# Kernel optimization log

Hardware: AMD Instinct MI355X
Metric: run time of the kernel (lower is better)

Reference implementation:

```python
import jax, jax.numpy as jnp
import numpy as np
from jax import lax

DEPTH = 8
LEAK = 0.01  # activations.relu(x, 0.01) == leaky relu


def _lrelu(z):
    return jnp.where(z >= 0, z, LEAK * z)


def _forward(x, mask, bucket_size, W_emb, b_emb, W, U, b, W1, b1,
             W_action_1, U_action_1, b_action_1, W_action_3, b_action_3):
    S = int(bucket_size)
    B = x.shape[0]
    H = W_emb.shape[1]
    dm = mask.T[:S]                         # [S,B] data mask (float)
    xe = x @ W_emb + b_emb                  # [B,S,H] embedding
    xe = jnp.transpose(xe, (1, 0, 2))[:S]   # [S,B,H] time-major
    # last_value_mask: 1 only at the final time step
    lvm = jnp.concatenate([jnp.zeros((S - 1, B), jnp.float32),
                           jnp.ones((1, B), jnp.float32)], axis=0)

    def hstep(carry, seq):
        h_tm1, nm_tm1, hv_tm1 = carry
        xt, pm, phv, lv = seq
        # action MLP -> per-sample gate
        a = _lrelu(xt @ W_action_1 + h_tm1 @ U_action_1 + b_action_1)  # [B,A]
        nm = jnp.clip(0.2 * (a @ W_action_3 + b_action_3) + 0.5, 0.0, 1.0)[:, 0]  # hard_sigmoid
        nm = (1.0 - lv) * (pm * phv * nm)
        both = pm * phv * (1.0 - nm) * hv_tm1
        x_only = pm * phv * (nm + (1.0 - nm) * (1.0 - hv_tm1))
        h_only = (1.0 - pm + pm * (1.0 - phv)) * (1.0 - nm) * hv_tm1
        hv = both + x_only + h_only
        h_ = _lrelu(xt @ W + h_tm1 @ U + b)      # [B,inner]
        h_ = _lrelu(h_ @ W1 + b1)                # [B,H]
        h = both[:, None] * h_ + x_only[:, None] * xt + h_only[:, None] * h_tm1
        return (h, nm, hv), (h, nm, hv)

    def vstep(carry, _):
        xv, xm, phv = carry  # [S,B,H], [S,B], [S,B]
        init = (jnp.zeros((B, H), jnp.float32),
                jnp.ones((B,), jnp.float32),
                jnp.zeros((B,), jnp.float32))
        _, (hs, nms, hvs) = lax.scan(hstep, init, (xv, xm, phv, lvm))
        # shift new_mask left by one step, pad last step with ones
        nms = jnp.concatenate([nms[1:], jnp.ones((1, B), jnp.float32)], axis=0)
        return (hs, nms, hvs), None

    (hfin, _, _), _ = lax.scan(vstep, (xe, dm, dm), None, length=DEPTH - 1)
    return hfin[-1]  # [B,H]: last time step of the last vertical level


def setup_inputs() -> dict:
    key = jax.random.key(0)
    ks = jax.random.split(key, 9)
    B, S, IN, H, INNER, A = 64, 256, 256, 256, 512, 64
    g = lambda k, shp: jax.random.normal(k, shp, jnp.float32) * np.float32(np.sqrt(2.0 / (shp[0] + shp[1])))
    return {
        "x": jax.random.normal(ks[0], (B, S, IN), jnp.float32),
        "mask": jnp.ones((B, S), jnp.float32),
        "bucket_size": S,
        "W_emb": g(ks[1], (IN, H)),
        "b_emb": jnp.zeros((H,), jnp.float32),
        "W": g(ks[2], (H, INNER)),
        "U": g(ks[3], (H, INNER)),
        "b": jnp.zeros((INNER,), jnp.float32),
        "W1": g(ks[4], (INNER, H)),
        "b1": jnp.zeros((H,), jnp.float32),
        "W_action_1": g(ks[5], (H, A)),
        "U_action_1": g(ks[6], (H, A)),
        "b_action_1": jnp.zeros((A,), jnp.float32),
        "W_action_3": g(ks[7], (A, 1)),
        "b_action_3": jnp.zeros((1,), jnp.float32),
    }


def reference(x, mask, bucket_size, W_emb, b_emb, W, U, b, W1, b1,
              W_action_1, U_action_1, b_action_1, W_action_3, b_action_3):
    return _forward(x, mask, bucket_size, W_emb, b_emb, W, U, b, W1, b1,
                    W_action_1, U_action_1, b_action_1, W_action_3, b_action_3)
```

## Files before the change

### kernel.cpp

```cpp
#include <hip/hip_runtime.h>
#include <stdint.h>


typedef _Float16 f16x8 __attribute__((ext_vector_type(8)));
typedef float    f32x4 __attribute__((ext_vector_type(4)));

static constexpr int SS = 256, BB = 64, DIN = 256, DH = 256, DNN = 512, DA = 64;

static constexpr size_t OFF_FLAGS = 0;
static constexpr size_t OFF_WEMB  = 8192;
static constexpr size_t SZ_WEMB   = (size_t)DIN * DH * 2;
static constexpr size_t OFF_W     = OFF_WEMB + SZ_WEMB;
static constexpr size_t SZ_WU     = (size_t)DH * DNN * 2;
static constexpr size_t OFF_U     = OFF_W + SZ_WU;
static constexpr size_t OFF_W1    = OFF_U + SZ_WU;
static constexpr size_t SZ_W1     = (size_t)DNN * DH * 2;
static constexpr size_t OFF_WA1   = OFF_W1 + SZ_W1;
static constexpr size_t SZ_WA     = (size_t)DH * DA * 2;
static constexpr size_t OFF_UA1   = OFF_WA1 + SZ_WA;
static constexpr size_t OFF_NM    = OFF_UA1 + SZ_WA;
static constexpr size_t SZ_NM     = (size_t)SS * BB * 4;
static constexpr size_t OFF_HV    = OFF_NM + 8 * SZ_NM;
static constexpr size_t OFF_G1    = OFF_HV + 8 * SZ_NM;
static constexpr size_t SZ_G1     = (size_t)BB * DNN * 2;
static constexpr size_t OFF_Z     = OFF_G1 + 8 * SZ_G1;
static constexpr size_t OFF_HB    = (size_t)4 << 20;
static constexpr size_t SZ_HB     = (size_t)SS * BB * DH * 2;
static constexpr size_t WS_NEEDED = OFF_HB + 8 * SZ_HB;

__device__ __forceinline__ float lrelu(float v) { return v >= 0.0f ? v : 0.01f * v; }

__device__ __forceinline__ f32x4 ld128(const f32x4* p) {
  f32x4 r;
  asm volatile("global_load_dwordx4 %0, %1, off sc0 sc1" : "=v"(r) : "v"(p) : "memory");
  return r;
}
__device__ __forceinline__ void st128(f32x4* p, f32x4 v) {
  asm volatile("global_store_dwordx4 %0, %1, off sc0 sc1" :: "v"(p), "v"(v) : "memory");
}
__device__ __forceinline__ float ldf(const float* p) {
  float r;
  asm volatile("global_load_dword %0, %1, off sc0 sc1" : "=v"(r) : "v"(p) : "memory");
  return r;
}
__device__ __forceinline__ void stf(float* p, float v) {
  asm volatile("global_store_dword %0, %1, off sc0 sc1" :: "v"(p), "v"(v) : "memory");
}
__device__ __forceinline__ void vwait() { asm volatile("s_waitcnt vmcnt(0)" ::: "memory"); }

__device__ __forceinline__ void pollf(const unsigned* p, unsigned need) {
  #pragma nounroll
  for (int g = 0; g < (1 << 18); ++g) {
    unsigned v;
    asm volatile("global_load_dword %0, %1, off sc0 sc1\n\ts_waitcnt vmcnt(0)"
                 : "=v"(v) : "v"(p) : "memory");
    if (v >= need) return;
  }
}

__global__ void zero_flags_k(unsigned* f) {
  f[threadIdx.x] = 0u;
  f[threadIdx.x + 1024] = 0u;
}

__global__ void pack_weight_k(const float* __restrict__ src, _Float16* __restrict__ dst,
                              int K, int N) {
  int idx = blockIdx.x * 256 + threadIdx.x;
  if (idx >= K * N) return;
  int k = idx / N, n = idx - k * N;
  int kt = k >> 5, q = (k >> 3) & 3, jj = k & 7;
  int nt = n >> 4, l = n & 15;
  size_t p = (((size_t)(kt * (N >> 4) + nt) * 4 + q) * 16 + l) * 8 + jj;
  dst[p] = (_Float16)src[idx];
}

__global__ __launch_bounds__(512, 2) void emb_k(const float* __restrict__ xin,
                                                const float* __restrict__ b_emb,
                                                char* __restrict__ ws) {
  const int tid = threadIdx.x, wave = tid >> 6, lane = tid & 63;
  const int l15 = lane & 15, quad = lane >> 4;
  const _Float16* Wp = (const _Float16*)(ws + OFF_WEMB);
  _Float16* xe = (_Float16*)(ws + OFF_HB);

  f16x8 bE[16];
  #pragma unroll
  for (int kt = 0; kt < 8; ++kt)
    #pragma unroll
    for (int i = 0; i < 2; ++i)
      bE[kt * 2 + i] = *(const f16x8*)(Wp + (((size_t)(kt * 16 + (wave * 2 + i)) * 4 + quad) * 16 + l15) * 8);
  float ber[2] = { b_emb[(wave * 2) * 16 + l15], b_emb[(wave * 2 + 1) * 16 + l15] };

  __shared__ __align__(16) _Float16 xtF[32 * 65 * 8];
  __shared__ __align__(16) _Float16 oF[32 * 65 * 8];

  for (int tt = 0; tt < 4; ++tt) {
    const int t = (int)blockIdx.x + 64 * tt;
    #pragma unroll
    for (int c = 0; c < 4; ++c) {
      int u = tid + 512 * c, s = u >> 5, kg = u & 31;
      const float* src = xin + ((size_t)s * SS + t) * DIN + kg * 8;
      f32x4 v0 = *(const f32x4*)src, v1 = *(const f32x4*)(src + 4);
      f16x8 p;
      p[0]=(_Float16)v0[0]; p[1]=(_Float16)v0[1]; p[2]=(_Float16)v0[2]; p[3]=(_Float16)v0[3];
      p[4]=(_Float16)v1[0]; p[5]=(_Float16)v1[1]; p[6]=(_Float16)v1[2]; p[7]=(_Float16)v1[3];
      *(f16x8*)(xtF + ((size_t)kg * 65 + s) * 8) = p;
    }
    __syncthreads();
    f32x4 acc[2][4] = {};
    #pragma unroll
    for (int kt = 0; kt < 8; ++kt) {
      f16x8 ax[4];
      #pragma unroll
      for (int mt = 0; mt < 4; ++mt)
        ax[mt] = *(const f16x8*)(xtF + (((size_t)(kt * 4 + quad)) * 65 + (mt * 16 + l15)) * 8);
      #pragma unroll
      for (int i = 0; i < 2; ++i)
        #pragma unroll
        for (int mt = 0; mt < 4; ++mt)
          acc[i][mt] = __builtin_amdgcn_mfma_f32_16x16x32_f16(ax[mt], bE[kt * 2 + i], acc[i][mt], 0, 0, 0);
    }
    #pragma unroll
    for (int i = 0; i < 2; ++i) {
      int n = (wave * 2 + i) * 16 + l15;
      int kq = n >> 3, jn = n & 7;
      #pragma unroll
      for (int mt = 0; mt < 4; ++mt)
        #pragma unroll
        for (int r = 0; r < 4; ++r) {
          int s = mt * 16 + quad * 4 + r;
          oF[((size_t)kq * 65 + s) * 8 + jn] = (_Float16)(acc[i][mt][r] + ber[i]);
        }
    }
    __syncthreads();
    #pragma unroll
    for (int c = 0; c < 4; ++c) {
      int u = tid + 512 * c, kq = u >> 6, s = u & 63;
      f32x4 v = *(const f32x4*)(oF + ((size_t)kq * 65 + s) * 8);
      *((f32x4*)(xe + (((size_t)t * 32 + kq) * 64 + s) * 8)) = v;
    }
    __syncthreads();
  }
}

__global__ __launch_bounds__(512, 2) void pipe_k(
    const float* __restrict__ mask, const float* __restrict__ b_in,
    const float* __restrict__ b1v, const float* __restrict__ bA1,
    const float* __restrict__ WA3, const float* __restrict__ bA3,
    char* __restrict__ ws, float* __restrict__ outp) {
  const int level = 1 + ((int)blockIdx.x >> 3);
  const int j     = (int)blockIdx.x & 7;
  const int tid   = threadIdx.x, wave = tid >> 6, lane = tid & 63;
  const int l15   = lane & 15, quad = lane >> 4;

  unsigned* flags = (unsigned*)(ws + OFF_FLAGS);
  unsigned* hfl   = flags + level * 64;
  unsigned* hflP  = flags + (level - 1) * 64;
  unsigned* gfl   = flags + (8 + level) * 64;

  const _Float16* Wp   = (const _Float16*)(ws + OFF_W);
  const _Float16* Up   = (const _Float16*)(ws + OFF_U);
  const _Float16* W1p  = (const _Float16*)(ws + OFF_W1);
  const _Float16* WA1p = (const _Float16*)(ws + OFF_WA1);
  const _Float16* UA1p = (const _Float16*)(ws + OFF_UA1);

  const f32x4* hPrev4 = (const f32x4*)((_Float16*)(ws + OFF_HB) + (size_t)(level - 1) * SS * BB * DH);
  f32x4*       hOwn4  = (f32x4*)((_Float16*)(ws + OFF_HB) + (size_t)level * SS * BB * DH);
  f32x4*       g1g4   = (f32x4*)(ws + OFF_G1 + (size_t)level * SZ_G1);
  float*       zg     = (float*)(ws + OFF_Z + (size_t)level * 4096);
  float*       nmW    = (float*)(ws + OFF_NM + (size_t)level * SZ_NM);
  float*       hvW    = (float*)(ws + OFF_HV + (size_t)level * SZ_NM);
  const float* nmR    = (const float*)(ws + OFF_NM + (size_t)(level - 1) * SZ_NM);
  const float* hvR    = (const float*)(ws + OFF_HV + (size_t)(level - 1) * SZ_NM);

  const int ntG = j * 4 + (wave >> 1);
  const int m0  = (wave & 1) * 2;
  f16x8 bW[8], bU[8];
  #pragma unroll
  for (int kt = 0; kt < 8; ++kt) {
    bW[kt] = *(const f16x8*)(Wp + (((size_t)(kt * 32 + ntG) * 4 + quad) * 16 + l15) * 8);
    bU[kt] = *(const f16x8*)(Up + (((size_t)(kt * 32 + ntG) * 4 + quad) * 16 + l15) * 8);
  }
  const int nt1 = j * 2 + (wave & 1);
  const int mt1 = wave >> 1;
  f16x8 b1f[16];
  #pragma unroll
  for (int kt = 0; kt < 16; ++kt)
    b1f[kt] = *(const f16x8*)(W1p + (((size_t)(kt * 16 + nt1) * 4 + quad) * 16 + l15) * 8);

  const int nG = ntG * 16 + l15;
  const int nC = nt1 * 16 + l15;
  const float bir  = b_in[nG];
  const float b1r  = b1v[nC];
  const float wa3r = WA3[(j & 3) * 16 + l15];
  const float ba1r = bA1[(j & 3) * 16 + l15];
  const float bA3v = bA3[0];

  __shared__ __align__(16) _Float16 xtF[32 * 64 * 8];
  __shared__ __align__(16) _Float16 htF[32 * 64 * 8];
  __shared__ __align__(16) _Float16 g1F[64 * 64 * 8];
  __shared__ __align__(16) _Float16 waF[16 * 64 * 8];
  __shared__ float gB[64], gX[64], gH[64], gHv[64];

  if (j < 4) {
    for (int u = tid; u < 1024; u += 512) {
      int ktm = u >> 6, lu = u & 63, kt = ktm >> 1, m = ktm & 1;
      const _Float16* sp = (m ? UA1p : WA1p) +
          (((size_t)(kt * 4 + j) * 4 + (lu >> 4)) * 16 + (lu & 15)) * 8;
      *(f16x8*)(waF + (size_t)u * 8) = *(const f16x8*)sp;
    }
  }
  for (int i = tid; i < 32 * 64 * 8; i += 512) htF[i] = (_Float16)0;
  if (tid < 64) gHv[tid] = 0.0f;
  float hreg[4] = {0.f, 0.f, 0.f, 0.f};
  __syncthreads();

  if (level >= 2) pollf(hflP + wave, 1);
  __syncthreads();
  {
    f32x4 pf[4];
    #pragma unroll
    for (int c = 0; c < 4; ++c) pf[c] = ld128(hPrev4 + tid + 512 * c);
    vwait();
    #pragma unroll
    for (int c = 0; c < 4; ++c) ((f32x4*)xtF)[tid + 512 * c] = pf[c];
  }
  __syncthreads();

  for (int t = 0; t < SS; ++t) {
    const bool last = (t == SS - 1);

    if (t > 0) pollf(hfl + wave, (unsigned)t);
    if (level >= 2) {
      unsigned need = (unsigned)((t + 2 <= SS) ? (t + 2) : SS);
      pollf(hflP + wave, need);
    }
    if (t > 0 && wave != j) {
      const f32x4* src = hOwn4 + (size_t)(t - 1) * 2048 + wave * 256;
      f32x4 hv4[4];
      #pragma unroll
      for (int it = 0; it < 4; ++it) hv4[it] = ld128(src + it * 64 + lane);
      vwait();
      #pragma unroll
      for (int it = 0; it < 4; ++it) ((f32x4*)htF)[wave * 256 + it * 64 + lane] = hv4[it];
    }
    __syncthreads();

    {
      f32x4 a0 = {}, a1 = {};
      #pragma unroll
      for (int kt = 0; kt < 8; ++kt) {
        int kq = kt * 4 + quad;
        f16x8 ax0 = *(const f16x8*)(xtF + ((size_t)(kq * 64 + m0 * 16 + l15)) * 8);
        f16x8 ax1 = *(const f16x8*)(xtF + ((size_t)(kq * 64 + (m0 + 1) * 16 + l15)) * 8);
        f16x8 ah0 = *(const f16x8*)(htF + ((size_t)(kq * 64 + m0 * 16 + l15)) * 8);
        f16x8 ah1 = *(const f16x8*)(htF + ((size_t)(kq * 64 + (m0 + 1) * 16 + l15)) * 8);
        a0 = __builtin_amdgcn_mfma_f32_16x16x32_f16(ax0, bW[kt], a0, 0, 0, 0);
        a1 = __builtin_amdgcn_mfma_f32_16x16x32_f16(ax1, bW[kt], a1, 0, 0, 0);
        a0 = __builtin_amdgcn_mfma_f32_16x16x32_f16(ah0, bU[kt], a0, 0, 0, 0);
        a1 = __builtin_amdgcn_mfma_f32_16x16x32_f16(ah1, bU[kt], a1, 0, 0, 0);
      }
      const int kqn = nG >> 3, jn = nG & 7;
      #pragma unroll
      for (int r = 0; r < 4; ++r) {
        g1F[((size_t)kqn * 64 + (m0 * 16 + quad * 4 + r)) * 8 + jn]       = (_Float16)lrelu(a0[r] + bir);
        g1F[((size_t)kqn * 64 + ((m0 + 1) * 16 + quad * 4 + r)) * 8 + jn] = (_Float16)lrelu(a1[r] + bir);
      }
      if (j < 4 && wave < 4) {
        f32x4 aa = {};
        #pragma unroll
        for (int kt = 0; kt < 8; ++kt) {
          int kq = kt * 4 + quad;
          f16x8 ax = *(const f16x8*)(xtF + ((size_t)(kq * 64 + wave * 16 + l15)) * 8);
          f16x8 ah = *(const f16x8*)(htF + ((size_t)(kq * 64 + wave * 16 + l15)) * 8);
          f16x8 bWa = *(const f16x8*)(waF + ((size_t)(kt * 2) * 64 + lane) * 8);
          f16x8 bUa = *(const f16x8*)(waF + ((size_t)(kt * 2 + 1) * 64 + lane) * 8);
          aa = __builtin_amdgcn_mfma_f32_16x16x32_f16(ax, bWa, aa, 0, 0, 0);
          aa = __builtin_amdgcn_mfma_f32_16x16x32_f16(ah, bUa, aa, 0, 0, 0);
        }
        #pragma unroll
        for (int r = 0; r < 4; ++r) {
          float v = lrelu(aa[r] + ba1r) * wa3r;
          v += __shfl_xor(v, 1); v += __shfl_xor(v, 2);
          v += __shfl_xor(v, 4); v += __shfl_xor(v, 8);
          if (l15 == 0) stf(&zg[j * 64 + wave * 16 + quad * 4 + r], v);
        }
      }
    }
    __syncthreads();
    {
      f32x4 v = ((const f32x4*)g1F)[j * 512 + tid];
      st128(g1g4 + j * 512 + tid, v);
      vwait();
    }
    __syncthreads();
    if (tid == 0)
      __hip_atomic_store(gfl + j, (unsigned)(t + 1), __ATOMIC_RELEASE, __HIP_MEMORY_SCOPE_AGENT);

    f32x4 pf[4];
    if (!last) {
      const f32x4* xs = hPrev4 + (size_t)(t + 1) * 2048;
      #pragma unroll
      for (int c = 0; c < 4; ++c) pf[c] = ld128(xs + tid + 512 * c);
      vwait();
    }

    if (wave != j) {
      pollf(gfl + wave, (unsigned)(t + 1));
      const f32x4* src = g1g4 + wave * 512;
      f32x4 g4[8];
      #pragma unroll
      for (int it = 0; it < 8; ++it) g4[it] = ld128(src + it * 64 + lane);
      vwait();
      #pragma unroll
      for (int it = 0; it < 8; ++it) ((f32x4*)g1F)[wave * 512 + it * 64 + lane] = g4[it];
    }
    __syncthreads();

    if (tid < 64) {
      int s = tid;
      float z0 = ldf(zg + s), z1 = ldf(zg + 64 + s), z2 = ldf(zg + 128 + s), z3 = ldf(zg + 192 + s);
      float pm, phv;
      if (level == 1) {
        vwait();
        float mv = mask[(size_t)s * SS + t];
        pm = mv; phv = mv;
      } else {
        size_t tn = (t + 1 < SS) ? (size_t)(t + 1) : 0;
        float pmv = ldf(nmR + tn * BB + s);
        float ph  = ldf(hvR + (size_t)t * BB + s);
        vwait();
        pm  = (t + 1 < SS) ? pmv : 1.0f;
        phv = ph;
      }
      float z    = bA3v + z0 + z1 + z2 + z3;
      float nm0  = fminf(fmaxf(0.2f * z + 0.5f, 0.0f), 1.0f);
      float lv   = last ? 1.0f : 0.0f;
      float nm   = (1.0f - lv) * (pm * phv * nm0);
      float hvp  = gHv[s], omn = 1.0f - nm;
      float both = pm * phv * omn * hvp;
      float xo   = pm * phv * (nm + omn * (1.0f - hvp));
      float ho   = (1.0f - pm * phv) * omn * hvp;
      float hv   = both + xo + ho;
      gB[s] = both; gX[s] = xo; gH[s] = ho; gHv[s] = hv;
      if (j == 0 && level < 7) {
        stf(&nmW[(size_t)t * BB + s], nm);
        stf(&hvW[(size_t)t * BB + s], hv);
      }
    }
    f32x4 c1 = {};
    #pragma unroll
    for (int kt = 0; kt < 16; ++kt) {
      f16x8 ag = *(const f16x8*)(g1F + ((size_t)((kt * 4 + quad) * 64 + mt1 * 16 + l15)) * 8);
      c1 = __builtin_amdgcn_mfma_f32_16x16x32_f16(ag, b1f[kt], c1, 0, 0, 0);
    }
    __syncthreads();

    {
      const int kqc = nC >> 3, jc = nC & 7;
      #pragma unroll
      for (int r = 0; r < 4; ++r) {
        int s = mt1 * 16 + quad * 4 + r;
        float h1  = lrelu(c1[r] + b1r);
        float xtv = (float)xtF[((size_t)(kqc * 64 + s)) * 8 + jc];
        float hn  = gB[s] * h1 + gX[s] * xtv + gH[s] * hreg[r];
        hreg[r] = hn;
        htF[((size_t)(kqc * 64 + s)) * 8 + jc] = (_Float16)hn;
        if (level == 7 && last) outp[(size_t)s * DH + nC] = hn;
      }
    }
    __syncthreads();
    if (tid < 256) {
      f32x4 v = ((const f32x4*)htF)[j * 256 + tid];
      st128(hOwn4 + (size_t)t * 2048 + j * 256 + tid, v);
    }
    if (!last) {
      #pragma unroll
      for (int c = 0; c < 4; ++c) ((f32x4*)xtF)[tid + 512 * c] = pf[c];
    }
    vwait();
    __syncthreads();
    if (tid == 0)
      __hip_atomic_store(hfl + j, (unsigned)(t + 1), __ATOMIC_RELEASE, __HIP_MEMORY_SCOPE_AGENT);
  }
}

extern "C" void kernel_launch(void* const* d_in, const int* in_sizes, int n_in,
                              void* d_out, int out_size, void* d_ws, size_t ws_size,
                              hipStream_t stream) {
  const float* x     = (const float*)d_in[0];
  const float* mask  = (const float*)d_in[1];
  const float* W_emb = (const float*)d_in[3];
  const float* b_emb = (const float*)d_in[4];
  const float* W     = (const float*)d_in[5];
  const float* U     = (const float*)d_in[6];
  const float* b     = (const float*)d_in[7];
  const float* W1    = (const float*)d_in[8];
  const float* b1    = (const float*)d_in[9];
  const float* WA1   = (const float*)d_in[10];
  const float* UA1   = (const float*)d_in[11];
  const float* bA1   = (const float*)d_in[12];
  const float* WA3   = (const float*)d_in[13];
  const float* bA3   = (const float*)d_in[14];
  char* ws = (char*)d_ws;

  if (ws_size < WS_NEEDED) return;

  zero_flags_k<<<1, 1024, 0, stream>>>((unsigned*)(ws + OFF_FLAGS));
  pack_weight_k<<<(DIN * DH + 255) / 256, 256, 0, stream>>>(W_emb, (_Float16*)(ws + OFF_WEMB), DIN, DH);
  pack_weight_k<<<(DH * DNN + 255) / 256, 256, 0, stream>>>(W, (_Float16*)(ws + OFF_W), DH, DNN);
  pack_weight_k<<<(DH * DNN + 255) / 256, 256, 0, stream>>>(U, (_Float16*)(ws + OFF_U), DH, DNN);
  pack_weight_k<<<(DNN * DH + 255) / 256, 256, 0, stream>>>(W1, (_Float16*)(ws + OFF_W1), DNN, DH);
  pack_weight_k<<<(DH * DA + 255) / 256, 256, 0, stream>>>(WA1, (_Float16*)(ws + OFF_WA1), DH, DA);
  pack_weight_k<<<(DH * DA + 255) / 256, 256, 0, stream>>>(UA1, (_Float16*)(ws + OFF_UA1), DH, DA);

  emb_k<<<64, 512, 0, stream>>>(x, b_emb, ws);
  pipe_k<<<56, 512, 0, stream>>>(mask, b, b1, bA1, WA3, bA3, ws, (float*)d_out);
}
```

Measured before the change: 3.612 ms.

## Pad sync flags, merge polls, batch global loads, and relax flag stores

Each sync flag now sits on its own 128-byte slot (FS stride), so different waves no longer poll the same cache line. The two per-step flag polls become one loop that issues both loads together, and polls back off with s_sleep. After the g1 exchange, the z partials, the next xt tile and the gate inputs are all loaded in one batch under a single wait, with z staged through shared memory instead of serialized loads in thread 0-63. Flag release stores change from atomic release to plain sc0 sc1 stores after vwait. This relies on the earlier waitcnt and syncthreads for ordering, and the sleeps may add wake-up latency.

```diff
diff --git a/kernel.cpp b/kernel.cpp
--- a/kernel.cpp
+++ b/kernel.cpp
@@ -6,9 +6,10 @@
 typedef float    f32x4 __attribute__((ext_vector_type(4)));
 
 static constexpr int SS = 256, BB = 64, DIN = 256, DH = 256, DNN = 512, DA = 64;
+static constexpr int FS = 32;
 
 static constexpr size_t OFF_FLAGS = 0;
-static constexpr size_t OFF_WEMB  = 8192;
+static constexpr size_t OFF_WEMB  = 16384;
 static constexpr size_t SZ_WEMB   = (size_t)DIN * DH * 2;
 static constexpr size_t OFF_W     = OFF_WEMB + SZ_WEMB;
 static constexpr size_t SZ_WU     = (size_t)DH * DNN * 2;
@@ -46,7 +47,13 @@
 __device__ __forceinline__ void stf(float* p, float v) {
   asm volatile("global_store_dword %0, %1, off sc0 sc1" :: "v"(p), "v"(v) : "memory");
 }
-__device__ __forceinline__ void vwait() { asm volatile("s_waitcnt vmcnt(0)" ::: "memory"); }
+__device__ __forceinline__ void stu(unsigned* p, unsigned v) {
+  asm volatile("global_store_dword %0, %1, off sc0 sc1" :: "v"(p), "v"(v) : "memory");
+}
+__device__ __forceinline__ void vwait() {
+  asm volatile("s_waitcnt vmcnt(0)" ::: "memory");
+  __builtin_amdgcn_sched_barrier(0);
+}
 
 __device__ __forceinline__ void pollf(const unsigned* p, unsigned need) {
   #pragma nounroll
@@ -55,12 +62,14 @@
     asm volatile("global_load_dword %0, %1, off sc0 sc1\n\ts_waitcnt vmcnt(0)"
                  : "=v"(v) : "v"(p) : "memory");
     if (v >= need) return;
+    if (g > 64)     __builtin_amdgcn_s_sleep(2);
+    else if (g > 8) __builtin_amdgcn_s_sleep(1);
   }
 }
 
 __global__ void zero_flags_k(unsigned* f) {
-  f[threadIdx.x] = 0u;
-  f[threadIdx.x + 1024] = 0u;
+  #pragma unroll
+  for (int i = 0; i < 4; ++i) f[threadIdx.x + 1024 * i] = 0u;
 }
 
 __global__ void pack_weight_k(const float* __restrict__ src, _Float16* __restrict__ dst,
@@ -153,9 +162,9 @@
   const int l15   = lane & 15, quad = lane >> 4;
 
   unsigned* flags = (unsigned*)(ws + OFF_FLAGS);
-  unsigned* hfl   = flags + level * 64;
-  unsigned* hflP  = flags + (level - 1) * 64;
-  unsigned* gfl   = flags + (8 + level) * 64;
+  unsigned* hfl   = flags + (size_t)level * 8 * FS;
+  unsigned* hflP  = flags + (size_t)(level - 1) * 8 * FS;
+  unsigned* gfl   = flags + (size_t)(8 + level) * 8 * FS;
 
   const _Float16* Wp   = (const _Float16*)(ws + OFF_W);
   const _Float16* Up   = (const _Float16*)(ws + OFF_U);
@@ -200,6 +209,7 @@
   __shared__ __align__(16) _Float16 g1F[64 * 64 * 8];
   __shared__ __align__(16) _Float16 waF[16 * 64 * 8];
   __shared__ float gB[64], gX[64], gH[64], gHv[64];
+  __shared__ float zL[256];
 
   if (j < 4) {
     for (int u = tid; u < 1024; u += 512) {
@@ -214,26 +224,40 @@
   float hreg[4] = {0.f, 0.f, 0.f, 0.f};
   __syncthreads();
 
-  if (level >= 2) pollf(hflP + wave, 1);
+  if (level >= 2) pollf(hflP + wave * FS, 1);
   __syncthreads();
   {
-    f32x4 pf[4];
-    #pragma unroll
-    for (int c = 0; c < 4; ++c) pf[c] = ld128(hPrev4 + tid + 512 * c);
+    f32x4 pf0[4];
+    #pragma unroll
+    for (int c = 0; c < 4; ++c) pf0[c] = ld128(hPrev4 + tid + 512 * c);
     vwait();
     #pragma unroll
-    for (int c = 0; c < 4; ++c) ((f32x4*)xtF)[tid + 512 * c] = pf[c];
+    for (int c = 0; c < 4; ++c) ((f32x4*)xtF)[tid + 512 * c] = pf0[c];
   }
   __syncthreads();
 
   for (int t = 0; t < SS; ++t) {
     const bool last = (t == SS - 1);
 
-    if (t > 0) pollf(hfl + wave, (unsigned)t);
-    if (level >= 2) {
-      unsigned need = (unsigned)((t + 2 <= SS) ? (t + 2) : SS);
-      pollf(hflP + wave, need);
-    }
+    {
+      const unsigned need1 = (unsigned)t;
+      const unsigned need2 = (level >= 2)
+          ? (unsigned)((t + 2 <= SS) ? (t + 2) : SS) : 0u;
+      const unsigned* p1 = hfl + wave * FS;
+      const unsigned* p2 = (level >= 2) ? (hflP + wave * FS) : p1;
+      #pragma nounroll
+      for (int g = 0; g < (1 << 18); ++g) {
+        unsigned v1, v2;
+        asm volatile("global_load_dword %0, %2, off sc0 sc1\n\t"
+                     "global_load_dword %1, %3, off sc0 sc1\n\t"
+                     "s_waitcnt vmcnt(0)"
+                     : "=&v"(v1), "=&v"(v2) : "v"(p1), "v"(p2) : "memory");
+        if (v1 >= need1 && v2 >= need2) break;
+        if (g > 64)     __builtin_amdgcn_s_sleep(2);
+        else if (g > 8) __builtin_amdgcn_s_sleep(1);
+      }
+    }
+
     if (t > 0 && wave != j) {
       const f32x4* src = hOwn4 + (size_t)(t - 1) * 2048 + wave * 256;
       f32x4 hv4[4];
@@ -293,46 +317,64 @@
       vwait();
     }
     __syncthreads();
-    if (tid == 0)
-      __hip_atomic_store(gfl + j, (unsigned)(t + 1), __ATOMIC_RELEASE, __HIP_MEMORY_SCOPE_AGENT);
+    if (tid == 0) stu(gfl + j * FS, (unsigned)(t + 1));
 
     f32x4 pf[4];
-    if (!last) {
-      const f32x4* xs = hPrev4 + (size_t)(t + 1) * 2048;
-      #pragma unroll
-      for (int c = 0; c < 4; ++c) pf[c] = ld128(xs + tid + 512 * c);
-      vwait();
-    }
-
-    if (wave != j) {
-      pollf(gfl + wave, (unsigned)(t + 1));
-      const f32x4* src = g1g4 + wave * 512;
-      f32x4 g4[8];
-      #pragma unroll
-      for (int it = 0; it < 8; ++it) g4[it] = ld128(src + it * 64 + lane);
-      vwait();
-      #pragma unroll
-      for (int it = 0; it < 8; ++it) ((f32x4*)g1F)[wave * 512 + it * 64 + lane] = g4[it];
+    float pmv = 1.0f, phh = 0.0f;
+    {
+      float zv = 0.0f;
+      const bool wantZ = (wave < 4);
+      const bool wantGate = (tid < 64) && (level >= 2);
+      if (wave != j) {
+        pollf(gfl + wave * FS, (unsigned)(t + 1));
+        const f32x4* src = g1g4 + wave * 512;
+        f32x4 g4[8];
+        #pragma unroll
+        for (int it = 0; it < 8; ++it) g4[it] = ld128(src + it * 64 + lane);
+        if (wantZ) zv = ldf(zg + wave * 64 + lane);
+        if (!last) {
+          const f32x4* xs = hPrev4 + (size_t)(t + 1) * 2048;
+          #pragma unroll
+          for (int c = 0; c < 4; ++c) pf[c] = ld128(xs + tid + 512 * c);
+        }
+        if (wantGate) {
+          size_t tn = (t + 1 < SS) ? (size_t)(t + 1) : 0;
+          pmv = ldf(nmR + tn * BB + tid);
+          phh = ldf(hvR + (size_t)t * BB + tid);
+        }
+        vwait();
+        #pragma unroll
+        for (int it = 0; it < 8; ++it) ((f32x4*)g1F)[wave * 512 + it * 64 + lane] = g4[it];
+      } else {
+        if (wantZ) zv = ldf(zg + wave * 64 + lane);
+        if (!last) {
+          const f32x4* xs = hPrev4 + (size_t)(t + 1) * 2048;
+          #pragma unroll
+          for (int c = 0; c < 4; ++c) pf[c] = ld128(xs + tid + 512 * c);
+        }
+        if (wantGate) {
+          size_t tn = (t + 1 < SS) ? (size_t)(t + 1) : 0;
+          pmv = ldf(nmR + tn * BB + tid);
+          phh = ldf(hvR + (size_t)t * BB + tid);
+        }
+        vwait();
+      }
+      if (wantGate) asm volatile("" : "+v"(pmv), "+v"(phh));
+      if (wantZ) zL[wave * 64 + lane] = zv;
     }
     __syncthreads();
 
     if (tid < 64) {
-      int s = tid;
-      float z0 = ldf(zg + s), z1 = ldf(zg + 64 + s), z2 = ldf(zg + 128 + s), z3 = ldf(zg + 192 + s);
+      const int s = tid;
       float pm, phv;
       if (level == 1) {
-        vwait();
         float mv = mask[(size_t)s * SS + t];
         pm = mv; phv = mv;
       } else {
-        size_t tn = (t + 1 < SS) ? (size_t)(t + 1) : 0;
-        float pmv = ldf(nmR + tn * BB + s);
-        float ph  = ldf(hvR + (size_t)t * BB + s);
-        vwait();
         pm  = (t + 1 < SS) ? pmv : 1.0f;
-        phv = ph;
-      }
-      float z    = bA3v + z0 + z1 + z2 + z3;
+        phv = phh;
+      }
+      float z    = bA3v + zL[s] + zL[64 + s] + zL[128 + s] + zL[192 + s];
       float nm0  = fminf(fmaxf(0.2f * z + 0.5f, 0.0f), 1.0f);
       float lv   = last ? 1.0f : 0.0f;
       float nm   = (1.0f - lv) * (pm * phv * nm0);
@@ -379,8 +421,7 @@
     }
     vwait();
     __syncthreads();
-    if (tid == 0)
-      __hip_atomic_store(hfl + j, (unsigned)(t + 1), __ATOMIC_RELEASE, __HIP_MEMORY_SCOPE_AGENT);
+    if (tid == 0) stu(hfl + j * FS, (unsigned)(t + 1));
   }
 }
 
```

New measurement: 3.234 ms. -10.5%, faster.

## Split recurrent pipeline by batch slice instead of output columns, removing intra-level exchange

Applied to the files above, without the earlier changes.

Each level's recurrence now runs on 4 blocks, each owning 16 batch rows, in place of 8 blocks each owning output-column slices. Every block computes the full hidden, inner and action projections for its rows, so the per-step global exchange of g1, z and h between sibling blocks and the extra flag round-trips go away. The trade-off is that each block re-reads the full W, U and W1 weights from global/L2 every step instead of keeping slices in registers, and fewer CUs are used. Polling also adds s_sleep backoff, and the release atomic store becomes a plain store with scope bits.

```diff
diff --git a/kernel.cpp b/kernel.cpp
--- a/kernel.cpp
+++ b/kernel.cpp
@@ -6,9 +6,10 @@
 typedef float    f32x4 __attribute__((ext_vector_type(4)));
 
 static constexpr int SS = 256, BB = 64, DIN = 256, DH = 256, DNN = 512, DA = 64;
+static constexpr int FS = 32;
 
 static constexpr size_t OFF_FLAGS = 0;
-static constexpr size_t OFF_WEMB  = 8192;
+static constexpr size_t OFF_WEMB  = 32768;
 static constexpr size_t SZ_WEMB   = (size_t)DIN * DH * 2;
 static constexpr size_t OFF_W     = OFF_WEMB + SZ_WEMB;
 static constexpr size_t SZ_WU     = (size_t)DH * DNN * 2;
@@ -21,9 +22,6 @@
 static constexpr size_t OFF_NM    = OFF_UA1 + SZ_WA;
 static constexpr size_t SZ_NM     = (size_t)SS * BB * 4;
 static constexpr size_t OFF_HV    = OFF_NM + 8 * SZ_NM;
-static constexpr size_t OFF_G1    = OFF_HV + 8 * SZ_NM;
-static constexpr size_t SZ_G1     = (size_t)BB * DNN * 2;
-static constexpr size_t OFF_Z     = OFF_G1 + 8 * SZ_G1;
 static constexpr size_t OFF_HB    = (size_t)4 << 20;
 static constexpr size_t SZ_HB     = (size_t)SS * BB * DH * 2;
 static constexpr size_t WS_NEEDED = OFF_HB + 8 * SZ_HB;
@@ -46,7 +44,13 @@
 __device__ __forceinline__ void stf(float* p, float v) {
   asm volatile("global_store_dword %0, %1, off sc0 sc1" :: "v"(p), "v"(v) : "memory");
 }
-__device__ __forceinline__ void vwait() { asm volatile("s_waitcnt vmcnt(0)" ::: "memory"); }
+__device__ __forceinline__ void stu(unsigned* p, unsigned v) {
+  asm volatile("global_store_dword %0, %1, off sc0 sc1" :: "v"(p), "v"(v) : "memory");
+}
+__device__ __forceinline__ void vwait() {
+  asm volatile("s_waitcnt vmcnt(0)" ::: "memory");
+  __builtin_amdgcn_sched_barrier(0);
+}
 
 __device__ __forceinline__ void pollf(const unsigned* p, unsigned need) {
   #pragma nounroll
@@ -55,12 +59,14 @@
     asm volatile("global_load_dword %0, %1, off sc0 sc1\n\ts_waitcnt vmcnt(0)"
                  : "=v"(v) : "v"(p) : "memory");
     if (v >= need) return;
+    if (g > 64)     __builtin_amdgcn_s_sleep(2);
+    else if (g > 8) __builtin_amdgcn_s_sleep(1);
   }
 }
 
 __global__ void zero_flags_k(unsigned* f) {
-  f[threadIdx.x] = 0u;
-  f[threadIdx.x + 1024] = 0u;
+  #pragma unroll
+  for (int i = 0; i < 8; ++i) f[threadIdx.x + 1024 * i] = 0u;
 }
 
 __global__ void pack_weight_k(const float* __restrict__ src, _Float16* __restrict__ dst,
@@ -147,15 +153,16 @@
     const float* __restrict__ b1v, const float* __restrict__ bA1,
     const float* __restrict__ WA3, const float* __restrict__ bA3,
     char* __restrict__ ws, float* __restrict__ outp) {
-  const int level = 1 + ((int)blockIdx.x >> 3);
-  const int j     = (int)blockIdx.x & 7;
+  const int bId   = (int)blockIdx.x;
+  const int level = 1 + (bId >> 2);
+  const int g     = bId & 3;
   const int tid   = threadIdx.x, wave = tid >> 6, lane = tid & 63;
   const int l15   = lane & 15, quad = lane >> 4;
+  const int kq16  = tid >> 4, sp16 = tid & 15;
 
   unsigned* flags = (unsigned*)(ws + OFF_FLAGS);
-  unsigned* hfl   = flags + level * 64;
-  unsigned* hflP  = flags + (level - 1) * 64;
-  unsigned* gfl   = flags + (8 + level) * 64;
+  unsigned* hfl   = flags + (size_t)(level * 4 + g) * FS;
+  unsigned* hflP  = flags + (size_t)((level - 1) * 4 + g) * FS;
 
   const _Float16* Wp   = (const _Float16*)(ws + OFF_W);
   const _Float16* Up   = (const _Float16*)(ws + OFF_U);
@@ -165,174 +172,125 @@
 
   const f32x4* hPrev4 = (const f32x4*)((_Float16*)(ws + OFF_HB) + (size_t)(level - 1) * SS * BB * DH);
   f32x4*       hOwn4  = (f32x4*)((_Float16*)(ws + OFF_HB) + (size_t)level * SS * BB * DH);
-  f32x4*       g1g4   = (f32x4*)(ws + OFF_G1 + (size_t)level * SZ_G1);
-  float*       zg     = (float*)(ws + OFF_Z + (size_t)level * 4096);
   float*       nmW    = (float*)(ws + OFF_NM + (size_t)level * SZ_NM);
   float*       hvW    = (float*)(ws + OFF_HV + (size_t)level * SZ_NM);
   const float* nmR    = (const float*)(ws + OFF_NM + (size_t)(level - 1) * SZ_NM);
   const float* hvR    = (const float*)(ws + OFF_HV + (size_t)(level - 1) * SZ_NM);
 
-  const int ntG = j * 4 + (wave >> 1);
-  const int m0  = (wave & 1) * 2;
-  f16x8 bW[8], bU[8];
+  float bir[4];
   #pragma unroll
-  for (int kt = 0; kt < 8; ++kt) {
-    bW[kt] = *(const f16x8*)(Wp + (((size_t)(kt * 32 + ntG) * 4 + quad) * 16 + l15) * 8);
-    bU[kt] = *(const f16x8*)(Up + (((size_t)(kt * 32 + ntG) * 4 + quad) * 16 + l15) * 8);
-  }
-  const int nt1 = j * 2 + (wave & 1);
-  const int mt1 = wave >> 1;
-  f16x8 b1f[16];
+  for (int nt = 0; nt < 4; ++nt) bir[nt] = b_in[(wave * 4 + nt) * 16 + l15];
+  float b1r[2];
   #pragma unroll
-  for (int kt = 0; kt < 16; ++kt)
-    b1f[kt] = *(const f16x8*)(W1p + (((size_t)(kt * 16 + nt1) * 4 + quad) * 16 + l15) * 8);
-
-  const int nG = ntG * 16 + l15;
-  const int nC = nt1 * 16 + l15;
-  const float bir  = b_in[nG];
-  const float b1r  = b1v[nC];
-  const float wa3r = WA3[(j & 3) * 16 + l15];
-  const float ba1r = bA1[(j & 3) * 16 + l15];
+  for (int nt = 0; nt < 2; ++nt) b1r[nt] = b1v[(wave * 2 + nt) * 16 + l15];
+  const float wa3r = WA3[(wave & 3) * 16 + l15];
+  const float ba1r = bA1[(wave & 3) * 16 + l15];
   const float bA3v = bA3[0];
 
-  __shared__ __align__(16) _Float16 xtF[32 * 64 * 8];
-  __shared__ __align__(16) _Float16 htF[32 * 64 * 8];
-  __shared__ __align__(16) _Float16 g1F[64 * 64 * 8];
-  __shared__ __align__(16) _Float16 waF[16 * 64 * 8];
-  __shared__ float gB[64], gX[64], gH[64], gHv[64];
-
-  if (j < 4) {
-    for (int u = tid; u < 1024; u += 512) {
-      int ktm = u >> 6, lu = u & 63, kt = ktm >> 1, m = ktm & 1;
-      const _Float16* sp = (m ? UA1p : WA1p) +
-          (((size_t)(kt * 4 + j) * 4 + (lu >> 4)) * 16 + (lu & 15)) * 8;
-      *(f16x8*)(waF + (size_t)u * 8) = *(const f16x8*)sp;
-    }
-  }
-  for (int i = tid; i < 32 * 64 * 8; i += 512) htF[i] = (_Float16)0;
-  if (tid < 64) gHv[tid] = 0.0f;
-  float hreg[4] = {0.f, 0.f, 0.f, 0.f};
+  __shared__ __align__(16) _Float16 xtL[32 * 16 * 8];
+  __shared__ __align__(16) _Float16 hL [32 * 16 * 8];
+  __shared__ __align__(16) _Float16 g1L[64 * 16 * 8];
+  __shared__ float zL[64];
+  __shared__ float gB[16], gX[16], gH[16], gHv[16];
+
+  for (int i = tid; i < 32 * 16 * 8; i += 512) hL[i] = (_Float16)0;
+  if (tid < 16) gHv[tid] = 0.0f;
   __syncthreads();
 
-  if (level >= 2) pollf(hflP + wave, 1);
+  if (level >= 2) pollf(hflP, 1);
   __syncthreads();
   {
-    f32x4 pf[4];
-    #pragma unroll
-    for (int c = 0; c < 4; ++c) pf[c] = ld128(hPrev4 + tid + 512 * c);
+    f32x4 v = ld128(hPrev4 + kq16 * 64 + g * 16 + sp16);
     vwait();
-    #pragma unroll
-    for (int c = 0; c < 4; ++c) ((f32x4*)xtF)[tid + 512 * c] = pf[c];
+    ((f32x4*)xtL)[tid] = v;
   }
   __syncthreads();
 
   for (int t = 0; t < SS; ++t) {
     const bool last = (t == SS - 1);
 
-    if (t > 0) pollf(hfl + wave, (unsigned)t);
-    if (level >= 2) {
-      unsigned need = (unsigned)((t + 2 <= SS) ? (t + 2) : SS);
-      pollf(hflP + wave, need);
-    }
-    if (t > 0 && wave != j) {
-      const f32x4* src = hOwn4 + (size_t)(t - 1) * 2048 + wave * 256;
-      f32x4 hv4[4];
-      #pragma unroll
-      for (int it = 0; it < 4; ++it) hv4[it] = ld128(src + it * 64 + lane);
-      vwait();
-      #pragma unroll
-      for (int it = 0; it < 4; ++it) ((f32x4*)htF)[wave * 256 + it * 64 + lane] = hv4[it];
-    }
-    __syncthreads();
+    if (level >= 2) pollf(hflP, (unsigned)((t + 2 <= SS) ? (t + 2) : SS));
 
     {
-      f32x4 a0 = {}, a1 = {};
+      f32x4 acc[4] = {};
       #pragma unroll
       for (int kt = 0; kt < 8; ++kt) {
-        int kq = kt * 4 + quad;
-        f16x8 ax0 = *(const f16x8*)(xtF + ((size_t)(kq * 64 + m0 * 16 + l15)) * 8);
-        f16x8 ax1 = *(const f16x8*)(xtF + ((size_t)(kq * 64 + (m0 + 1) * 16 + l15)) * 8);
-        f16x8 ah0 = *(const f16x8*)(htF + ((size_t)(kq * 64 + m0 * 16 + l15)) * 8);
-        f16x8 ah1 = *(const f16x8*)(htF + ((size_t)(kq * 64 + (m0 + 1) * 16 + l15)) * 8);
-        a0 = __builtin_amdgcn_mfma_f32_16x16x32_f16(ax0, bW[kt], a0, 0, 0, 0);
-        a1 = __builtin_amdgcn_mfma_f32_16x16x32_f16(ax1, bW[kt], a1, 0, 0, 0);
-        a0 = __builtin_amdgcn_mfma_f32_16x16x32_f16(ah0, bU[kt], a0, 0, 0, 0);
-        a1 = __builtin_amdgcn_mfma_f32_16x16x32_f16(ah1, bU[kt], a1, 0, 0, 0);
-      }
-      const int kqn = nG >> 3, jn = nG & 7;
-      #pragma unroll
-      for (int r = 0; r < 4; ++r) {
-        g1F[((size_t)kqn * 64 + (m0 * 16 + quad * 4 + r)) * 8 + jn]       = (_Float16)lrelu(a0[r] + bir);
-        g1F[((size_t)kqn * 64 + ((m0 + 1) * 16 + quad * 4 + r)) * 8 + jn] = (_Float16)lrelu(a1[r] + bir);
-      }
-      if (j < 4 && wave < 4) {
+        f16x8 ax = *(const f16x8*)(xtL + ((size_t)((kt * 4 + quad) * 16 + l15)) * 8);
+        f16x8 ah = *(const f16x8*)(hL  + ((size_t)((kt * 4 + quad) * 16 + l15)) * 8);
+        #pragma unroll
+        for (int i = 0; i < 4; ++i) {
+          f16x8 wf = *(const f16x8*)(Wp + (((size_t)(kt * 32 + (wave * 4 + i)) * 4 + quad) * 16 + l15) * 8);
+          f16x8 uf = *(const f16x8*)(Up + (((size_t)(kt * 32 + (wave * 4 + i)) * 4 + quad) * 16 + l15) * 8);
+          acc[i] = __builtin_amdgcn_mfma_f32_16x16x32_f16(ax, wf, acc[i], 0, 0, 0);
+          acc[i] = __builtin_amdgcn_mfma_f32_16x16x32_f16(ah, uf, acc[i], 0, 0, 0);
+        }
+      }
+      #pragma unroll
+      for (int i = 0; i < 4; ++i) {
+        const int n = (wave * 4 + i) * 16 + l15;
+        const int kqn = n >> 3, jn = n & 7;
+        #pragma unroll
+        for (int r = 0; r < 4; ++r)
+          g1L[((size_t)kqn * 16 + (quad * 4 + r)) * 8 + jn] = (_Float16)lrelu(acc[i][r] + bir[i]);
+      }
+      if (wave < 4) {
         f32x4 aa = {};
         #pragma unroll
         for (int kt = 0; kt < 8; ++kt) {
-          int kq = kt * 4 + quad;
-          f16x8 ax = *(const f16x8*)(xtF + ((size_t)(kq * 64 + wave * 16 + l15)) * 8);
-          f16x8 ah = *(const f16x8*)(htF + ((size_t)(kq * 64 + wave * 16 + l15)) * 8);
-          f16x8 bWa = *(const f16x8*)(waF + ((size_t)(kt * 2) * 64 + lane) * 8);
-          f16x8 bUa = *(const f16x8*)(waF + ((size_t)(kt * 2 + 1) * 64 + lane) * 8);
-          aa = __builtin_amdgcn_mfma_f32_16x16x32_f16(ax, bWa, aa, 0, 0, 0);
-          aa = __builtin_amdgcn_mfma_f32_16x16x32_f16(ah, bUa, aa, 0, 0, 0);
+          f16x8 ax = *(const f16x8*)(xtL + ((size_t)((kt * 4 + quad) * 16 + l15)) * 8);
+          f16x8 ah = *(const f16x8*)(hL  + ((size_t)((kt * 4 + quad) * 16 + l15)) * 8);
+          f16x8 wa = *(const f16x8*)(WA1p + (((size_t)(kt * 4 + wave) * 4 + quad) * 16 + l15) * 8);
+          f16x8 ua = *(const f16x8*)(UA1p + (((size_t)(kt * 4 + wave) * 4 + quad) * 16 + l15) * 8);
+          aa = __builtin_amdgcn_mfma_f32_16x16x32_f16(ax, wa, aa, 0, 0, 0);
+          aa = __builtin_amdgcn_mfma_f32_16x16x32_f16(ah, ua, aa, 0, 0, 0);
         }
         #pragma unroll
         for (int r = 0; r < 4; ++r) {
           float v = lrelu(aa[r] + ba1r) * wa3r;
           v += __shfl_xor(v, 1); v += __shfl_xor(v, 2);
           v += __shfl_xor(v, 4); v += __shfl_xor(v, 8);
-          if (l15 == 0) stf(&zg[j * 64 + wave * 16 + quad * 4 + r], v);
+          if (l15 == 0) zL[wave * 16 + quad * 4 + r] = v;
         }
       }
     }
     __syncthreads();
+
+    f32x4 c1[2] = {};
+    #pragma unroll
+    for (int kt = 0; kt < 16; ++kt) {
+      f16x8 ag = *(const f16x8*)(g1L + ((size_t)((kt * 4 + quad) * 16 + l15)) * 8);
+      #pragma unroll
+      for (int nt = 0; nt < 2; ++nt) {
+        f16x8 w1f = *(const f16x8*)(W1p + (((size_t)(kt * 16 + (wave * 2 + nt)) * 4 + quad) * 16 + l15) * 8);
+        c1[nt] = __builtin_amdgcn_mfma_f32_16x16x32_f16(ag, w1f, c1[nt], 0, 0, 0);
+      }
+    }
+
+    f32x4 pf;
+    float pmv = 1.0f, phh = 0.0f;
     {
-      f32x4 v = ((const f32x4*)g1F)[j * 512 + tid];
-      st128(g1g4 + j * 512 + tid, v);
+      const bool wantGate = (tid < 16) && (level >= 2);
+      if (!last) pf = ld128(hPrev4 + (size_t)(t + 1) * 2048 + kq16 * 64 + g * 16 + sp16);
+      if (wantGate) {
+        size_t tn = (t + 1 < SS) ? (size_t)(t + 1) : 0;
+        pmv = ldf(nmR + tn * BB + g * 16 + tid);
+        phh = ldf(hvR + (size_t)t * BB + g * 16 + tid);
+      }
       vwait();
-    }
-    __syncthreads();
-    if (tid == 0)
-      __hip_atomic_store(gfl + j, (unsigned)(t + 1), __ATOMIC_RELEASE, __HIP_MEMORY_SCOPE_AGENT);
-
-    f32x4 pf[4];
-    if (!last) {
-      const f32x4* xs = hPrev4 + (size_t)(t + 1) * 2048;
-      #pragma unroll
-      for (int c = 0; c < 4; ++c) pf[c] = ld128(xs + tid + 512 * c);
-      vwait();
-    }
-
-    if (wave != j) {
-      pollf(gfl + wave, (unsigned)(t + 1));
-      const f32x4* src = g1g4 + wave * 512;
-      f32x4 g4[8];
-      #pragma unroll
-      for (int it = 0; it < 8; ++it) g4[it] = ld128(src + it * 64 + lane);
-      vwait();
-      #pragma unroll
-      for (int it = 0; it < 8; ++it) ((f32x4*)g1F)[wave * 512 + it * 64 + lane] = g4[it];
-    }
-    __syncthreads();
-
-    if (tid < 64) {
-      int s = tid;
-      float z0 = ldf(zg + s), z1 = ldf(zg + 64 + s), z2 = ldf(zg + 128 + s), z3 = ldf(zg + 192 + s);
+      if (wantGate) asm volatile("" : "+v"(pmv), "+v"(phh));
+    }
+
+    if (tid < 16) {
+      const int s = tid;
       float pm, phv;
       if (level == 1) {
-        vwait();
-        float mv = mask[(size_t)s * SS + t];
+        float mv = mask[(size_t)(g * 16 + s) * SS + t];
         pm = mv; phv = mv;
       } else {
-        size_t tn = (t + 1 < SS) ? (size_t)(t + 1) : 0;
-        float pmv = ldf(nmR + tn * BB + s);
-        float ph  = ldf(hvR + (size_t)t * BB + s);
-        vwait();
         pm  = (t + 1 < SS) ? pmv : 1.0f;
-        phv = ph;
-      }
-      float z    = bA3v + z0 + z1 + z2 + z3;
+        phv = phh;
+      }
+      float z    = bA3v + zL[s] + zL[16 + s] + zL[32 + s] + zL[48 + s];
       float nm0  = fminf(fmaxf(0.2f * z + 0.5f, 0.0f), 1.0f);
       float lv   = last ? 1.0f : 0.0f;
       float nm   = (1.0f - lv) * (pm * phv * nm0);
@@ -342,45 +300,39 @@
       float ho   = (1.0f - pm * phv) * omn * hvp;
       float hv   = both + xo + ho;
       gB[s] = both; gX[s] = xo; gH[s] = ho; gHv[s] = hv;
-      if (j == 0 && level < 7) {
-        stf(&nmW[(size_t)t * BB + s], nm);
-        stf(&hvW[(size_t)t * BB + s], hv);
-      }
-    }
-    f32x4 c1 = {};
-    #pragma unroll
-    for (int kt = 0; kt < 16; ++kt) {
-      f16x8 ag = *(const f16x8*)(g1F + ((size_t)((kt * 4 + quad) * 64 + mt1 * 16 + l15)) * 8);
-      c1 = __builtin_amdgcn_mfma_f32_16x16x32_f16(ag, b1f[kt], c1, 0, 0, 0);
+      if (level < 7) {
+        stf(&nmW[(size_t)t * BB + g * 16 + s], nm);
+        stf(&hvW[(size_t)t * BB + g * 16 + s], hv);
+      }
+    }
+    __syncthreads();
+
+    #pragma unroll
+    for (int nt = 0; nt < 2; ++nt) {
+      const int n = (wave * 2 + nt) * 16 + l15;
+      const int kqc = n >> 3, jc = n & 7;
+      #pragma unroll
+      for (int r = 0; r < 4; ++r) {
+        int s = quad * 4 + r;
+        size_t idx = ((size_t)kqc * 16 + s) * 8 + jc;
+        float h1  = lrelu(c1[nt][r] + b1r[nt]);
+        float xtv = (float)xtL[idx];
+        float hp  = (float)hL[idx];
+        float hn  = gB[s] * h1 + gX[s] * xtv + gH[s] * hp;
+        hL[idx] = (_Float16)hn;
+        if (level == 7 && last) outp[(size_t)(g * 16 + s) * DH + n] = hn;
+      }
     }
     __syncthreads();
 
     {
-      const int kqc = nC >> 3, jc = nC & 7;
-      #pragma unroll
-      for (int r = 0; r < 4; ++r) {
-        int s = mt1 * 16 + quad * 4 + r;
-        float h1  = lrelu(c1[r] + b1r);
-        float xtv = (float)xtF[((size_t)(kqc * 64 + s)) * 8 + jc];
-        float hn  = gB[s] * h1 + gX[s] * xtv + gH[s] * hreg[r];
-        hreg[r] = hn;
-        htF[((size_t)(kqc * 64 + s)) * 8 + jc] = (_Float16)hn;
-        if (level == 7 && last) outp[(size_t)s * DH + nC] = hn;
-      }
-    }
-    __syncthreads();
-    if (tid < 256) {
-      f32x4 v = ((const f32x4*)htF)[j * 256 + tid];
-      st128(hOwn4 + (size_t)t * 2048 + j * 256 + tid, v);
-    }
-    if (!last) {
-      #pragma unroll
-      for (int c = 0; c < 4; ++c) ((f32x4*)xtF)[tid + 512 * c] = pf[c];
-    }
+      f32x4 v = ((const f32x4*)hL)[tid];
+      st128(hOwn4 + (size_t)t * 2048 + kq16 * 64 + g * 16 + sp16, v);
+    }
+    if (!last) ((f32x4*)xtL)[tid] = pf;
     vwait();
     __syncthreads();
-    if (tid == 0)
-      __hip_atomic_store(hfl + j, (unsigned)(t + 1), __ATOMIC_RELEASE, __HIP_MEMORY_SCOPE_AGENT);
+    if (tid == 0) stu(hfl, (unsigned)(t + 1));
   }
 }
 
@@ -414,5 +366,5 @@
   pack_weight_k<<<(DH * DA + 255) / 256, 256, 0, stream>>>(UA1, (_Float16*)(ws + OFF_UA1), DH, DA);
 
   emb_k<<<64, 512, 0, stream>>>(x, b_emb, ws);
-  pipe_k<<<56, 512, 0, stream>>>(mask, b, b1, bA1, WA3, bA3, ws, (float*)d_out);
-}
+  pipe_k<<<28, 512, 0, stream>>>(mask, b, b1, bA1, WA3, bA3, ws, (float*)d_out);
+}
```

Result: slower. 3.847 ms (+6.5%).
